# Optimization experiments

Measured on AMD Instinct MI355X. Metric: run time of the kernel, lower is better.

The kernel has to match this reference:

```python
import jax, jax.numpy as jnp
import numpy as np

B, S, D = 8, 4096, 1024       # batch, seq_len, d_model
WIN = 257                     # window_size (odd): keys [i-128, i+128]
HALF = WIN // 2               # 128
BL = 256                      # block length for banded attention (BL >= HALF, S % BL == 0)


def setup_inputs() -> dict:
    key = jax.random.key(0)
    ks = jax.random.split(key, 7)
    s = 0.02
    return {
        "x":  jax.random.normal(ks[0], (B, S, D), jnp.float32),
        "Wq": jax.random.normal(ks[1], (D, D), jnp.float32) * s,
        "bq": jnp.zeros((D,), jnp.float32),
        "Wk": jax.random.normal(ks[2], (D, D), jnp.float32) * s,
        "bk": jnp.zeros((D,), jnp.float32),
        "Wv": jax.random.normal(ks[3], (D, D), jnp.float32) * s,
        "bv": jnp.zeros((D,), jnp.float32),
    }


def _blockify(t, nb):
    # t: [B, S, D] -> [B, nb, 3*BL, D]; for block b, keys from blocks b-1, b, b+1 (zero-padded at edges)
    b, s, d = t.shape
    tp = jnp.pad(t, ((0, 0), (BL, BL), (0, 0)))
    tb = tp.reshape(b, nb + 2, BL, d)
    return jnp.concatenate([tb[:, :-2], tb[:, 1:-1], tb[:, 2:]], axis=2)


def _local_attention(q, k, v):
    # Faithful vectorized form of the per-token sliding-window loop:
    # for each i: keys/values from [max(0, i-HALF), min(S, i+HALF+1)), scaled-dot softmax.
    b, s, d = q.shape
    nb = s // BL
    qb = q.reshape(b, nb, BL, d)
    kb = _blockify(k, nb)                          # [B, nb, 3BL, D]
    vb = _blockify(v, nb)
    scale = 1.0 / np.sqrt(d).astype(np.float32)    # d_model ** 0.5 (scaled_dot)
    scores = jnp.einsum('bnqd,bnkd->bnqk', qb, kb) * scale  # [B, nb, BL, 3BL]

    blk = jnp.arange(nb)[:, None, None]
    r = jnp.arange(BL)[None, :, None]
    c = jnp.arange(3 * BL)[None, None, :]
    i = blk * BL + r                               # global query position
    j = (blk - 1) * BL + c                         # global key position
    rel = j - i
    valid = (rel >= -HALF) & (rel <= HALF) & (j >= 0) & (j < s)  # [nb, BL, 3BL]

    scores = jnp.where(valid[None], scores, -jnp.inf)
    weights = jax.nn.softmax(scores, axis=-1)
    out = jnp.einsum('bnqk,bnkd->bnqd', weights, vb)
    return out.reshape(b, s, d)


def reference(x, Wq, bq, Wk, bk, Wv, bv) -> jnp.ndarray:
    q = x @ Wq + bq
    k = x @ Wk + bk
    v = x @ Wv + bv
    return _local_attention(q, k, v)
```

## Files before the change

kernel.cpp:

```cpp
#include <hip/hip_runtime.h>
#include <hip/hip_fp16.h>
#include <cstdint>


#define DEV __device__ __forceinline__

typedef _Float16 f16x8 __attribute__((ext_vector_type(8)));
typedef _Float16 f16x4 __attribute__((ext_vector_type(4)));
typedef float    f32x4 __attribute__((ext_vector_type(4)));

DEV _Float16 f2h(float f) { return (_Float16)f; }

DEV void gl16(const void* g, void* l) {
  __builtin_amdgcn_global_load_lds(
      (const __attribute__((address_space(1))) void*)(uintptr_t)g,
      (__attribute__((address_space(3))) void*)(uintptr_t)l, 16, 0, 0);
}

#define MFMA16(a, b, c) __builtin_amdgcn_mfma_f32_16x16x32_f16((a), (b), (c), 0, 0, 0)

__global__ __launch_bounds__(256) void k_cvt_x(const float* __restrict__ x,
                                               _Float16* __restrict__ xh) {
  size_t i = ((size_t)blockIdx.x * 256 + threadIdx.x) * 8;
  float4 f0 = *(const float4*)(x + i);
  float4 f1 = *(const float4*)(x + i + 4);
  f16x8 o;
  o[0] = f2h(f0.x); o[1] = f2h(f0.y); o[2] = f2h(f0.z); o[3] = f2h(f0.w);
  o[4] = f2h(f1.x); o[5] = f2h(f1.y); o[6] = f2h(f1.z); o[7] = f2h(f1.w);
  *(f16x8*)(xh + i) = o;
}

__global__ __launch_bounds__(256) void k_cvt_w(const float* __restrict__ Wq,
                                               const float* __restrict__ Wk,
                                               const float* __restrict__ Wv,
                                               _Float16* __restrict__ wt) {
  __shared__ float tile[64][65];
  const int z = blockIdx.z;
  const int n0 = blockIdx.x * 64, k0 = blockIdx.y * 64;
  const float* W = (z == 0) ? Wq : (z == 1) ? Wk : Wv;
  const int tid = threadIdx.x;
  const int r0 = tid >> 4;
  const int c4 = (tid & 15) * 4;
#pragma unroll
  for (int rr = 0; rr < 4; ++rr) {
    int r = r0 + rr * 16;
    float4 v = *(const float4*)(W + (size_t)(k0 + r) * 1024 + n0 + c4);
    tile[r][c4 + 0] = v.x; tile[r][c4 + 1] = v.y;
    tile[r][c4 + 2] = v.z; tile[r][c4 + 3] = v.w;
  }
  __syncthreads();
  _Float16* out = wt + (size_t)z * 1048576;
#pragma unroll
  for (int rr = 0; rr < 4; ++rr) {
    int n = r0 + rr * 16;
    f16x4 o;
#pragma unroll
    for (int jj = 0; jj < 4; ++jj) o[jj] = f2h(tile[c4 + jj][n]);
    *(f16x4*)(out + (size_t)(n0 + n) * 1024 + k0 + c4) = o;
  }
}

__global__ __launch_bounds__(512, 2) void k_gemm_qkv(
    const _Float16* __restrict__ xh, const _Float16* __restrict__ wt,
    const float* __restrict__ bq, const float* __restrict__ bk,
    const float* __restrict__ bv, _Float16* __restrict__ qh,
    _Float16* __restrict__ kh, _Float16* __restrict__ v8) {
  __shared__ _Float16 L[65536];

  const int bid = blockIdx.x;
  const int wg = (bid & 7) * 192 + (bid >> 3);
  const int mt = wg / 12, nt = wg % 12;
  const int gm0 = mt * 256;
  const int gn0 = nt * 256;

  const int tid = threadIdx.x;
  const int w = tid >> 6, l = tid & 63;
  const int ln = l & 15, quad = l >> 4;
  const int wm = w >> 2, wn = w & 3;
  const int lr = l >> 3;
  const int kc = ((l & 7) ^ lr) * 8;
  const int swz = ln & 7;

  auto stageA = [&](int it, int h) {
    const _Float16* src =
        xh + (size_t)(gm0 + h * 128 + w * 8 + lr) * 1024 + it * 64 + kc;
    _Float16* dst = L + (it & 1) * 32768 + (h * 128 + w * 8) * 64;
    gl16(src, dst);
    gl16(src + 64 * 1024, dst + 64 * 64);
  };
  auto stageB = [&](int it, int h) {
    const _Float16* src =
        wt + (size_t)(gn0 + h * 128 + w * 8 + lr) * 1024 + it * 64 + kc;
    _Float16* dst = L + (it & 1) * 32768 + 16384 + (h * 128 + w * 8) * 64;
    gl16(src, dst);
    gl16(src + 64 * 1024, dst + 64 * 64);
  };

#define RD(base, r, ko) \
  (*(const f16x8*)((base) + (size_t)(r) * 64 + (((ko) ^ swz) * 8)))

  f32x4 acc[8][4] = {};
  f16x8 aA[2][4], bb0[2][2], bb1[2][2];

  stageA(0, 0); stageA(0, 1); stageB(0, 0); stageB(0, 1);
  stageB(1, 0); stageB(1, 1);
  asm volatile("s_waitcnt vmcnt(4)" ::: "memory");
  __builtin_amdgcn_s_barrier();

#pragma unroll 2
  for (int t = 0; t < 16; ++t) {
    const _Float16* Ab = L + (t & 1) * 32768;
    const _Float16* Bb = Ab + 16384;
    const int rA = wm * 128 + ln;
    const int rB = wn * 64 + ln;

#pragma unroll
    for (int i = 0; i < 4; ++i) {
      aA[0][i] = RD(Ab, rA + i * 16, quad);
      aA[1][i] = RD(Ab, rA + i * 16, quad + 4);
    }
#pragma unroll
    for (int j = 0; j < 2; ++j) {
      bb0[0][j] = RD(Bb, rB + j * 16, quad);
      bb0[1][j] = RD(Bb, rB + j * 16, quad + 4);
    }
    if (t + 1 < 16) stageA(t + 1, 0);
    __builtin_amdgcn_s_barrier();
    asm volatile("s_waitcnt lgkmcnt(0)" ::: "memory");
    __builtin_amdgcn_sched_barrier(0);
    __builtin_amdgcn_s_setprio(1);
#pragma unroll
    for (int s = 0; s < 2; ++s)
#pragma unroll
      for (int i = 0; i < 4; ++i)
#pragma unroll
        for (int j = 0; j < 2; ++j)
          acc[i][j] = MFMA16(aA[s][i], bb0[s][j], acc[i][j]);
    __builtin_amdgcn_s_setprio(0);
    __builtin_amdgcn_s_barrier();

#pragma unroll
    for (int j = 0; j < 2; ++j) {
      bb1[0][j] = RD(Bb, rB + 32 + j * 16, quad);
      bb1[1][j] = RD(Bb, rB + 32 + j * 16, quad + 4);
    }
    if (t + 1 < 16) stageA(t + 1, 1);
    __builtin_amdgcn_s_barrier();
    asm volatile("s_waitcnt lgkmcnt(0)" ::: "memory");
    __builtin_amdgcn_sched_barrier(0);
    __builtin_amdgcn_s_setprio(1);
#pragma unroll
    for (int s = 0; s < 2; ++s)
#pragma unroll
      for (int i = 0; i < 4; ++i)
#pragma unroll
        for (int j = 0; j < 2; ++j)
          acc[i][2 + j] = MFMA16(aA[s][i], bb1[s][j], acc[i][2 + j]);
    __builtin_amdgcn_s_setprio(0);
    __builtin_amdgcn_s_barrier();

#pragma unroll
    for (int i = 0; i < 4; ++i) {
      aA[0][i] = RD(Ab, rA + 64 + i * 16, quad);
      aA[1][i] = RD(Ab, rA + 64 + i * 16, quad + 4);
    }
    if (t + 2 < 16) stageB(t + 2, 0);
    __builtin_amdgcn_s_barrier();
    asm volatile("s_waitcnt lgkmcnt(0)" ::: "memory");
    __builtin_amdgcn_sched_barrier(0);
    __builtin_amdgcn_s_setprio(1);
#pragma unroll
    for (int s = 0; s < 2; ++s)
#pragma unroll
      for (int i = 0; i < 4; ++i)
#pragma unroll
        for (int j = 0; j < 2; ++j)
          acc[4 + i][2 + j] = MFMA16(aA[s][i], bb1[s][j], acc[4 + i][2 + j]);
    __builtin_amdgcn_s_setprio(0);
    __builtin_amdgcn_s_barrier();

    if (t + 2 < 16) stageB(t + 2, 1);
    __builtin_amdgcn_s_setprio(1);
#pragma unroll
    for (int s = 0; s < 2; ++s)
#pragma unroll
      for (int i = 0; i < 4; ++i)
#pragma unroll
        for (int j = 0; j < 2; ++j)
          acc[4 + i][j] = MFMA16(aA[s][i], bb0[s][j], acc[4 + i][j]);
    __builtin_amdgcn_s_setprio(0);
    if (t + 2 < 16)
      asm volatile("s_waitcnt vmcnt(4)" ::: "memory");
    else
      asm volatile("s_waitcnt vmcnt(0)" ::: "memory");
    __builtin_amdgcn_s_barrier();
  }
#undef RD

  const int z2 = gn0 >> 10;
  const int colz = (gn0 & 1023) + wn * 64;
  const int row0 = gm0 + wm * 128;
  if (z2 != 2) {
    const float* bias = z2 ? bk : bq;
    _Float16* outp = z2 ? kh : qh;
#pragma unroll
    for (int j = 0; j < 4; ++j) {
      float bb = bias[colz + j * 16 + ln];
#pragma unroll
      for (int i = 0; i < 8; ++i) {
        int row = row0 + i * 16 + quad * 4;
        size_t base = (size_t)row * 1024 + colz + j * 16 + ln;
#pragma unroll
        for (int r = 0; r < 4; ++r)
          outp[base + (size_t)r * 1024] = f2h(acc[i][j][r] + bb);
      }
    }
  } else {
#pragma unroll
    for (int j = 0; j < 4; ++j) {
      float bb = bv[colz + j * 16 + ln];
#pragma unroll
      for (int i = 0; i < 8; ++i) {
        int rr = row0 + i * 16 + quad * 4;
        int col = colz + j * 16 + ln;
        f16x4 o;
#pragma unroll
        for (int r = 0; r < 4; ++r) o[r] = f2h(acc[i][j][r] + bb);
        *(f16x4*)(v8 + (size_t)(rr >> 3) * 8192 + (size_t)col * 8 + (rr & 7)) = o;
      }
    }
  }
}

__global__ __launch_bounds__(256) void k_scores(const _Float16* __restrict__ qh,
                                                const _Float16* __restrict__ kh,
                                                _Float16* __restrict__ ph) {
  __shared__ _Float16 lQ[64 * 64];
  __shared__ _Float16 lK[320 * 64];
  const int t = blockIdx.x, b = blockIdx.y;
  const int i0 = t * 64, k0 = i0 - 128;
  const int tid = threadIdx.x, w = tid >> 6, l = tid & 63;
  const int ln = l & 15, quad = l >> 4;
  const _Float16* qrow = qh + (size_t)b * 4096 * 1024;
  const _Float16* krow = kh + (size_t)b * 4096 * 1024;
  const int kc = (((l & 7) ^ (l >> 3)) * 8);
  const int swz = ln & 7;

  f32x4 acc[20] = {};

  for (int it = 0; it < 16; ++it) {
#pragma unroll
    for (int c = 0; c < 2; ++c) {
      int cid = w * 2 + c;
      int rl = cid * 8 + (l >> 3);
      gl16(qrow + (size_t)(i0 + rl) * 1024 + it * 64 + kc, lQ + cid * 512);
    }
#pragma unroll
    for (int c = 0; c < 10; ++c) {
      int cid = w * 10 + c;
      int rl = cid * 8 + (l >> 3);
      int gr = k0 + rl;
      gr = min(max(gr, 0), 4095);
      gl16(krow + (size_t)gr * 1024 + it * 64 + kc, lK + cid * 512);
    }
    __builtin_amdgcn_s_waitcnt(0);
    __syncthreads();
#pragma unroll
    for (int kk = 0; kk < 64; kk += 32) {
      f16x8 a = *(const f16x8*)(lQ + (w * 16 + ln) * 64 +
                                (((kk >> 3) + quad) ^ swz) * 8);
#pragma unroll
      for (int j = 0; j < 20; ++j) {
        f16x8 bf = *(const f16x8*)(lK + (j * 16 + ln) * 64 +
                                   (((kk >> 3) + quad) ^ swz) * 8);
        acc[j] = MFMA16(a, bf, acc[j]);
      }
    }
    __syncthreads();
  }

  const float scale = 0.03125f;
  float mrow[4] = {-1e30f, -1e30f, -1e30f, -1e30f};
#pragma unroll
  for (int j = 0; j < 20; ++j) {
    int jc = k0 + j * 16 + ln;
    bool cval = (jc >= 0) && (jc < 4096);
#pragma unroll
    for (int r = 0; r < 4; ++r) {
      int i = i0 + w * 16 + quad * 4 + r;
      int rel = jc - i;
      bool val = cval && (rel >= -128) && (rel <= 128);
      float s = val ? acc[j][r] * scale : -1e30f;
      acc[j][r] = s;
      mrow[r] = fmaxf(mrow[r], s);
    }
  }
#pragma unroll
  for (int r = 0; r < 4; ++r)
#pragma unroll
    for (int m = 1; m < 16; m <<= 1) mrow[r] = fmaxf(mrow[r], __shfl_xor(mrow[r], m));
  float sum[4] = {0.f, 0.f, 0.f, 0.f};
#pragma unroll
  for (int j = 0; j < 20; ++j)
#pragma unroll
    for (int r = 0; r < 4; ++r) {
      float e = __builtin_exp2f((acc[j][r] - mrow[r]) * 1.44269504f);
      acc[j][r] = e;
      sum[r] += e;
    }
#pragma unroll
  for (int r = 0; r < 4; ++r) {
#pragma unroll
    for (int m = 1; m < 16; m <<= 1) sum[r] += __shfl_xor(sum[r], m);
    sum[r] = 1.0f / sum[r];
  }
  _Float16* pt = ph + (size_t)(b * 64 + t) * 64 * 320;
#pragma unroll
  for (int j = 0; j < 20; ++j)
#pragma unroll
    for (int r = 0; r < 4; ++r)
      pt[(size_t)(w * 16 + quad * 4 + r) * 320 + j * 16 + ln] = f2h(acc[j][r] * sum[r]);
}

__global__ __launch_bounds__(256) void k_pv(const _Float16* __restrict__ ph,
                                            const _Float16* __restrict__ v8,
                                            float* __restrict__ out) {
  __shared__ _Float16 lP[64 * 40];
  __shared__ _Float16 lV[4 * 256 * 8];
  const int nc = blockIdx.x, t = blockIdx.y, b = blockIdx.z;
  const int n0 = nc * 256;
  const int tid = threadIdx.x, w = tid >> 6, l = tid & 63;
  const int ln = l & 15, quad = l >> 4;
  const _Float16* pt = ph + (size_t)(b * 64 + t) * 64 * 320;
  const _Float16* vb = v8 + (size_t)b * 4194304;
  const int k0 = t * 64 - 128;

  f32x4 acc[16] = {};

  for (int it = 0; it < 10; ++it) {
    int kk = it * 32;
    if (it) __syncthreads();
    {
      int row = tid >> 2, ch = tid & 3;
      f16x8 d = *(const f16x8*)(pt + (size_t)row * 320 + kk + ch * 8);
      *(f16x8*)(lP + row * 40 + ch * 8) = d;
    }
#pragma unroll
    for (int c = 0; c < 4; ++c) {
      int nloc = w * 64 + l;
      int g = ((k0 + kk) >> 3) + c;
      g = min(max(g, 0), 511);
      gl16(vb + (size_t)g * 8192 + (size_t)(n0 + nloc) * 8, lV + (c * 256 + w * 64) * 8);
    }
    __builtin_amdgcn_s_waitcnt(0);
    __syncthreads();
    f16x8 a = *(const f16x8*)(lP + (w * 16 + ln) * 40 + quad * 8);
#pragma unroll
    for (int j = 0; j < 16; ++j) {
      f16x8 bv = *(const f16x8*)(lV + (quad * 256 + j * 16 + ln) * 8);
      acc[j] = MFMA16(a, bv, acc[j]);
    }
  }

#pragma unroll
  for (int j = 0; j < 16; ++j) {
    int col = n0 + j * 16 + ln;
    int row = t * 64 + w * 16 + quad * 4;
    size_t base = ((size_t)b * 4096 + row) * 1024 + col;
#pragma unroll
    for (int r = 0; r < 4; ++r) out[base + (size_t)r * 1024] = acc[j][r];
  }
}

extern "C" void kernel_launch(void* const* d_in, const int* in_sizes, int n_in,
                              void* d_out, int out_size, void* d_ws, size_t ws_size,
                              hipStream_t stream) {
  const float* x  = (const float*)d_in[0];
  const float* Wq = (const float*)d_in[1];
  const float* bq = (const float*)d_in[2];
  const float* Wk = (const float*)d_in[3];
  const float* bk = (const float*)d_in[4];
  const float* Wv = (const float*)d_in[5];
  const float* bv = (const float*)d_in[6];
  float* out = (float*)d_out;

  _Float16* ws = (_Float16*)d_ws;
  _Float16* xh = ws;
  _Float16* wt = ws + 33554432;
  _Float16* qh = ws + 36700160;
  _Float16* kh = ws + 70254592;
  _Float16* v8 = ws + 103809024;
  _Float16* ph = ws;

  k_cvt_x<<<16384, 256, 0, stream>>>(x, xh);
  k_cvt_w<<<dim3(16, 16, 3), 256, 0, stream>>>(Wq, Wk, Wv, wt);
  k_gemm_qkv<<<dim3(1536), 512, 0, stream>>>(xh, wt, bq, bk, bv, qh, kh, v8);
  k_scores<<<dim3(64, 8), 256, 0, stream>>>(qh, kh, ph);
  k_pv<<<dim3(4, 64, 8), 256, 0, stream>>>(ph, v8, out);
}
```

Measured before the change: 570.6 us.

## Enlarge attention tiles to 128 queries with double-buffered loads and swizzled P

The scores kernel now processes 128 query rows per block with 512 threads. It loads Q and K tiles through double-buffered LDS and reduces softmax max and sum across waves through shared memory. The PV kernel loads the whole swizzled P tile into LDS once and loops over output-column chunks with double-buffered V staging, instead of reloading P per column block. The aim is to cut redundant key/P traffic and hide load latency, at the cost of large LDS use, one block per CU, and hand-written vmcnt waits that are fragile.

```diff
diff --git a/kernel.cpp b/kernel.cpp
--- a/kernel.cpp
+++ b/kernel.cpp
@@ -232,143 +232,232 @@
   }
 }
 
-__global__ __launch_bounds__(256) void k_scores(const _Float16* __restrict__ qh,
+__global__ __launch_bounds__(512) void k_scores(const _Float16* __restrict__ qh,
                                                 const _Float16* __restrict__ kh,
                                                 _Float16* __restrict__ ph) {
-  __shared__ _Float16 lQ[64 * 64];
-  __shared__ _Float16 lK[320 * 64];
+  __shared__ _Float16 lQ[2][128 * 64];
+  __shared__ _Float16 lK[2][384 * 64];
+  __shared__ float redM[4][128];
+  __shared__ float redS[4][128];
   const int t = blockIdx.x, b = blockIdx.y;
-  const int i0 = t * 64, k0 = i0 - 128;
+  const int i0 = t * 128, k0 = i0 - 128;
   const int tid = threadIdx.x, w = tid >> 6, l = tid & 63;
   const int ln = l & 15, quad = l >> 4;
+  const int wm2 = w >> 2, wn4 = w & 3;
   const _Float16* qrow = qh + (size_t)b * 4096 * 1024;
   const _Float16* krow = kh + (size_t)b * 4096 * 1024;
-  const int kc = (((l & 7) ^ (l >> 3)) * 8);
+  const int kc = ((l & 7) ^ (l >> 3)) * 8;
   const int swz = ln & 7;
 
-  f32x4 acc[20] = {};
-
-  for (int it = 0; it < 16; ++it) {
+  auto stage = [&](int it) {
+    int buf = it & 1;
 #pragma unroll
     for (int c = 0; c < 2; ++c) {
       int cid = w * 2 + c;
       int rl = cid * 8 + (l >> 3);
-      gl16(qrow + (size_t)(i0 + rl) * 1024 + it * 64 + kc, lQ + cid * 512);
-    }
-#pragma unroll
-    for (int c = 0; c < 10; ++c) {
-      int cid = w * 10 + c;
+      gl16(qrow + (size_t)(i0 + rl) * 1024 + it * 64 + kc, &lQ[buf][cid * 512]);
+    }
+#pragma unroll
+    for (int c = 0; c < 6; ++c) {
+      int cid = w * 6 + c;
       int rl = cid * 8 + (l >> 3);
-      int gr = k0 + rl;
-      gr = min(max(gr, 0), 4095);
-      gl16(krow + (size_t)gr * 1024 + it * 64 + kc, lK + cid * 512);
-    }
-    __builtin_amdgcn_s_waitcnt(0);
-    __syncthreads();
-#pragma unroll
-    for (int kk = 0; kk < 64; kk += 32) {
-      f16x8 a = *(const f16x8*)(lQ + (w * 16 + ln) * 64 +
-                                (((kk >> 3) + quad) ^ swz) * 8);
-#pragma unroll
-      for (int j = 0; j < 20; ++j) {
-        f16x8 bf = *(const f16x8*)(lK + (j * 16 + ln) * 64 +
-                                   (((kk >> 3) + quad) ^ swz) * 8);
-        acc[j] = MFMA16(a, bf, acc[j]);
+      int gr = min(max(k0 + rl, 0), 4095);
+      gl16(krow + (size_t)gr * 1024 + it * 64 + kc, &lK[buf][cid * 512]);
+    }
+  };
+
+  f32x4 s[4][6] = {};
+
+  stage(0);
+  asm volatile("s_waitcnt vmcnt(0)" ::: "memory");
+  __builtin_amdgcn_s_barrier();
+
+  for (int it = 0; it < 16; ++it) {
+    int buf = it & 1;
+    if (it + 1 < 16) stage(it + 1);
+    f16x8 af[2][4], bf[2][6];
+#pragma unroll
+    for (int i = 0; i < 4; ++i) {
+      int r = wm2 * 64 + i * 16 + ln;
+      af[0][i] = *(const f16x8*)(&lQ[buf][r * 64 + ((quad ^ swz) * 8)]);
+      af[1][i] = *(const f16x8*)(&lQ[buf][r * 64 + (((quad + 4) ^ swz) * 8)]);
+    }
+#pragma unroll
+    for (int j = 0; j < 6; ++j) {
+      int r = wn4 * 96 + j * 16 + ln;
+      bf[0][j] = *(const f16x8*)(&lK[buf][r * 64 + ((quad ^ swz) * 8)]);
+      bf[1][j] = *(const f16x8*)(&lK[buf][r * 64 + (((quad + 4) ^ swz) * 8)]);
+    }
+    asm volatile("s_waitcnt lgkmcnt(0)" ::: "memory");
+    __builtin_amdgcn_sched_barrier(0);
+    __builtin_amdgcn_s_setprio(1);
+#pragma unroll
+    for (int ss = 0; ss < 2; ++ss)
+#pragma unroll
+      for (int i = 0; i < 4; ++i)
+#pragma unroll
+        for (int j = 0; j < 6; ++j)
+          s[i][j] = MFMA16(af[ss][i], bf[ss][j], s[i][j]);
+    __builtin_amdgcn_s_setprio(0);
+    asm volatile("s_waitcnt vmcnt(0)" ::: "memory");
+    __builtin_amdgcn_s_barrier();
+  }
+
+  const float scale = 0.03125f;
+  float mrow[4][4];
+#pragma unroll
+  for (int i = 0; i < 4; ++i)
+#pragma unroll
+    for (int r = 0; r < 4; ++r) mrow[i][r] = -1e30f;
+#pragma unroll
+  for (int j = 0; j < 6; ++j) {
+    int jc = k0 + wn4 * 96 + j * 16 + ln;
+    bool cval = (jc >= 0) && (jc < 4096);
+#pragma unroll
+    for (int i = 0; i < 4; ++i)
+#pragma unroll
+      for (int r = 0; r < 4; ++r) {
+        int iq = i0 + wm2 * 64 + i * 16 + quad * 4 + r;
+        int rel = jc - iq;
+        bool val = cval && (rel >= -128) && (rel <= 128);
+        float sc = val ? s[i][j][r] * scale : -1e30f;
+        s[i][j][r] = sc;
+        mrow[i][r] = fmaxf(mrow[i][r], sc);
       }
-    }
-    __syncthreads();
-  }
-
-  const float scale = 0.03125f;
-  float mrow[4] = {-1e30f, -1e30f, -1e30f, -1e30f};
-#pragma unroll
-  for (int j = 0; j < 20; ++j) {
-    int jc = k0 + j * 16 + ln;
-    bool cval = (jc >= 0) && (jc < 4096);
+  }
+#pragma unroll
+  for (int i = 0; i < 4; ++i)
+#pragma unroll
+    for (int r = 0; r < 4; ++r)
+#pragma unroll
+      for (int m = 1; m < 16; m <<= 1)
+        mrow[i][r] = fmaxf(mrow[i][r], __shfl_xor(mrow[i][r], m));
+  if (ln == 0) {
+#pragma unroll
+    for (int i = 0; i < 4; ++i)
+#pragma unroll
+      for (int r = 0; r < 4; ++r)
+        redM[wn4][wm2 * 64 + i * 16 + quad * 4 + r] = mrow[i][r];
+  }
+  __syncthreads();
+  float mf[4][4];
+#pragma unroll
+  for (int i = 0; i < 4; ++i)
 #pragma unroll
     for (int r = 0; r < 4; ++r) {
-      int i = i0 + w * 16 + quad * 4 + r;
-      int rel = jc - i;
-      bool val = cval && (rel >= -128) && (rel <= 128);
-      float s = val ? acc[j][r] * scale : -1e30f;
-      acc[j][r] = s;
-      mrow[r] = fmaxf(mrow[r], s);
-    }
-  }
-#pragma unroll
-  for (int r = 0; r < 4; ++r)
-#pragma unroll
-    for (int m = 1; m < 16; m <<= 1) mrow[r] = fmaxf(mrow[r], __shfl_xor(mrow[r], m));
-  float sum[4] = {0.f, 0.f, 0.f, 0.f};
-#pragma unroll
-  for (int j = 0; j < 20; ++j)
+      int row = wm2 * 64 + i * 16 + quad * 4 + r;
+      mf[i][r] = fmaxf(fmaxf(redM[0][row], redM[1][row]),
+                       fmaxf(redM[2][row], redM[3][row]));
+    }
+  float srow[4][4] = {};
+#pragma unroll
+  for (int j = 0; j < 6; ++j)
+#pragma unroll
+    for (int i = 0; i < 4; ++i)
+#pragma unroll
+      for (int r = 0; r < 4; ++r) {
+        float e = __builtin_exp2f((s[i][j][r] - mf[i][r]) * 1.44269504f);
+        s[i][j][r] = e;
+        srow[i][r] += e;
+      }
+#pragma unroll
+  for (int i = 0; i < 4; ++i)
+#pragma unroll
+    for (int r = 0; r < 4; ++r)
+#pragma unroll
+      for (int m = 1; m < 16; m <<= 1) srow[i][r] += __shfl_xor(srow[i][r], m);
+  if (ln == 0) {
+#pragma unroll
+    for (int i = 0; i < 4; ++i)
+#pragma unroll
+      for (int r = 0; r < 4; ++r)
+        redS[wn4][wm2 * 64 + i * 16 + quad * 4 + r] = srow[i][r];
+  }
+  __syncthreads();
+  float inv[4][4];
+#pragma unroll
+  for (int i = 0; i < 4; ++i)
 #pragma unroll
     for (int r = 0; r < 4; ++r) {
-      float e = __builtin_exp2f((acc[j][r] - mrow[r]) * 1.44269504f);
-      acc[j][r] = e;
-      sum[r] += e;
-    }
-#pragma unroll
-  for (int r = 0; r < 4; ++r) {
-#pragma unroll
-    for (int m = 1; m < 16; m <<= 1) sum[r] += __shfl_xor(sum[r], m);
-    sum[r] = 1.0f / sum[r];
-  }
-  _Float16* pt = ph + (size_t)(b * 64 + t) * 64 * 320;
-#pragma unroll
-  for (int j = 0; j < 20; ++j)
-#pragma unroll
-    for (int r = 0; r < 4; ++r)
-      pt[(size_t)(w * 16 + quad * 4 + r) * 320 + j * 16 + ln] = f2h(acc[j][r] * sum[r]);
-}
-
-__global__ __launch_bounds__(256) void k_pv(const _Float16* __restrict__ ph,
+      int row = wm2 * 64 + i * 16 + quad * 4 + r;
+      inv[i][r] = 1.0f / (redS[0][row] + redS[1][row] + redS[2][row] + redS[3][row]);
+    }
+  _Float16* pt = ph + (size_t)(b * 32 + t) * 128 * 384;
+#pragma unroll
+  for (int j = 0; j < 6; ++j) {
+    int col = wn4 * 96 + j * 16 + ln;
+    int oct = col >> 3, e = col & 7;
+#pragma unroll
+    for (int i = 0; i < 4; ++i)
+#pragma unroll
+      for (int r = 0; r < 4; ++r) {
+        int row = wm2 * 64 + i * 16 + quad * 4 + r;
+        pt[row * 384 + ((oct ^ (row & 7)) << 3) + e] = f2h(s[i][j][r] * inv[i][r]);
+      }
+  }
+}
+
+__global__ __launch_bounds__(512) void k_pv(const _Float16* __restrict__ ph,
                                             const _Float16* __restrict__ v8,
                                             float* __restrict__ out) {
-  __shared__ _Float16 lP[64 * 40];
-  __shared__ _Float16 lV[4 * 256 * 8];
-  const int nc = blockIdx.x, t = blockIdx.y, b = blockIdx.z;
-  const int n0 = nc * 256;
+  __shared__ _Float16 lP[128 * 384];
+  __shared__ _Float16 lV[2][48 * 32 * 8];
+  const int t = blockIdx.x, b = blockIdx.y;
   const int tid = threadIdx.x, w = tid >> 6, l = tid & 63;
   const int ln = l & 15, quad = l >> 4;
-  const _Float16* pt = ph + (size_t)(b * 64 + t) * 64 * 320;
+  const int wq = w >> 1, wn2 = w & 1;
+  const _Float16* pt = ph + (size_t)(b * 32 + t) * 128 * 384;
   const _Float16* vb = v8 + (size_t)b * 4194304;
-  const int k0 = t * 64 - 128;
-
-  f32x4 acc[16] = {};
-
-  for (int it = 0; it < 10; ++it) {
-    int kk = it * 32;
-    if (it) __syncthreads();
-    {
-      int row = tid >> 2, ch = tid & 3;
-      f16x8 d = *(const f16x8*)(pt + (size_t)row * 320 + kk + ch * 8);
-      *(f16x8*)(lP + row * 40 + ch * 8) = d;
-    }
-#pragma unroll
-    for (int c = 0; c < 4; ++c) {
-      int nloc = w * 64 + l;
-      int g = ((k0 + kk) >> 3) + c;
-      g = min(max(g, 0), 511);
-      gl16(vb + (size_t)g * 8192 + (size_t)(n0 + nloc) * 8, lV + (c * 256 + w * 64) * 8);
-    }
-    __builtin_amdgcn_s_waitcnt(0);
-    __syncthreads();
-    f16x8 a = *(const f16x8*)(lP + (w * 16 + ln) * 40 + quad * 8);
-#pragma unroll
-    for (int j = 0; j < 16; ++j) {
-      f16x8 bv = *(const f16x8*)(lV + (quad * 256 + j * 16 + ln) * 8);
-      acc[j] = MFMA16(a, bv, acc[j]);
-    }
-  }
-
-#pragma unroll
-  for (int j = 0; j < 16; ++j) {
-    int col = n0 + j * 16 + ln;
-    int row = t * 64 + w * 16 + quad * 4;
-    size_t base = ((size_t)b * 4096 + row) * 1024 + col;
-#pragma unroll
-    for (int r = 0; r < 4; ++r) out[base + (size_t)r * 1024] = acc[j][r];
+  const int g0 = (t * 128 - 128) >> 3;
+
+  auto stageV = [&](int c) {
+    int buf = c & 1;
+    int n0 = c * 32;
+#pragma unroll
+    for (int cc = 0; cc < 3; ++cc) {
+      int ob = w * 6 + cc * 2;
+      int oct = ob + (l >> 5);
+      int g = min(max(g0 + oct, 0), 511);
+      gl16(vb + (size_t)g * 8192 + (size_t)(n0 + (l & 31)) * 8,
+           &lV[buf][ob * 256]);
+    }
+  };
+
+  #pragma unroll
+  for (int c = 0; c < 12; ++c)
+    gl16(pt + ((size_t)(c * 512 + w * 64 + l)) * 8, &lP[(c * 512 + w * 64) * 8]);
+  stageV(0);
+  stageV(1);
+  asm volatile("s_waitcnt vmcnt(3)" ::: "memory");
+  __builtin_amdgcn_s_barrier();
+
+  for (int c = 0; c < 32; ++c) {
+    int buf = c & 1;
+    if (c + 1 < 32) stageV(c + 1);
+    f32x4 acc[2] = {};
+#pragma unroll
+    for (int ks = 0; ks < 12; ++ks) {
+      int o = ks * 4 + quad;
+      int rA0 = wq * 32 + ln;
+      int rA1 = rA0 + 16;
+      f16x8 a0 = *(const f16x8*)(&lP[rA0 * 384 + ((o ^ (rA0 & 7)) << 3)]);
+      f16x8 a1 = *(const f16x8*)(&lP[rA1 * 384 + ((o ^ (rA1 & 7)) << 3)]);
+      f16x8 bv = *(const f16x8*)(&lV[buf][(o * 32 + wn2 * 16 + ln) * 8]);
+      acc[0] = MFMA16(a0, bv, acc[0]);
+      acc[1] = MFMA16(a1, bv, acc[1]);
+    }
+    int col = c * 32 + wn2 * 16 + ln;
+#pragma unroll
+    for (int i = 0; i < 2; ++i) {
+      int row = t * 128 + wq * 32 + i * 16 + quad * 4;
+      size_t base = ((size_t)b * 4096 + row) * 1024 + col;
+#pragma unroll
+      for (int r = 0; r < 4; ++r) out[base + (size_t)r * 1024] = acc[i][r];
+    }
+    if (c + 1 < 32) {
+      asm volatile("s_waitcnt vmcnt(8)" ::: "memory");
+      __builtin_amdgcn_s_barrier();
+    }
   }
 }
 
@@ -395,6 +484,6 @@
   k_cvt_x<<<16384, 256, 0, stream>>>(x, xh);
   k_cvt_w<<<dim3(16, 16, 3), 256, 0, stream>>>(Wq, Wk, Wv, wt);
   k_gemm_qkv<<<dim3(1536), 512, 0, stream>>>(xh, wt, bq, bk, bv, qh, kh, v8);
-  k_scores<<<dim3(64, 8), 256, 0, stream>>>(qh, kh, ph);
-  k_pv<<<dim3(4, 64, 8), 256, 0, stream>>>(ph, v8, out);
-}
+  k_scores<<<dim3(32, 8), 512, 0, stream>>>(qh, kh, ph);
+  k_pv<<<dim3(32, 8), 512, 0, stream>>>(ph, v8, out);
+}
```

Measured after the change: 556.4 us. 1.03x faster.
